# Performance work log

Measured on AMD Instinct MI355X. Metric: run time of the kernel, lower is better.

## Reference

```python
import jax, jax.numpy as jnp
import numpy as np

D_K = 64  # matches init_kwargs d_k


def setup_inputs() -> dict:
    key = jax.random.key(0)
    k0, k1, k2, k3 = jax.random.split(key, 4)
    B, H, TW, L, D = 4, 8, 20, 256, 64
    q = jax.random.normal(k0, (B, H, TW, D), dtype=jnp.float32)
    k = jax.random.normal(k1, (B, H, L, D), dtype=jnp.float32)
    v = jax.random.normal(k2, (B, H, L, D), dtype=jnp.float32)
    bias = jax.random.normal(k3, (B, L, H, TW, L), dtype=jnp.float32)
    return {"q": q, "k": k, "v": v, "bias": bias}


def reference(q, k, v, bias):
    # q: [B,H,TW,D]; k,v: [B,H,L,D]; bias: [B,L,H,TW,L]
    B, H, TW, D = q.shape
    L = k.shape[2]
    # The torch code expands q over the L axis before matmul with k^T; since
    # QK^T does not depend on that axis, compute it once and broadcast.
    scores = jnp.einsum('bhwd,bhld->bhwl', q, k) / jnp.sqrt(jnp.asarray(D_K, q.dtype))
    # weight: [B,L,H,TW,L]; dropout-before-softmax is identity in eval mode
    w = jax.nn.softmax(scores[:, None, :, :, :] + bias, axis=-1)
    # transpose(1,2).view(B,H,L*TW,L) @ v, then transpose(1,2).view(B,L*TW,H*D)
    attn = jnp.einsum('blhwk,bhkd->blwhd', w, v)  # [B,L,TW,H,D]
    return attn.reshape(B, L * TW, H * D)
```

## Files before the change

kernel.cpp:

```cpp
#include <hip/hip_runtime.h>
#include <hip/hip_bf16.h>

#define NB 4
#define NH 8
#define NW 20
#define NL 256
#define ND 64
#define ROWGRPS 40

typedef __attribute__((ext_vector_type(8))) short bf16x8;
typedef __attribute__((ext_vector_type(4))) short short4v;
typedef __attribute__((ext_vector_type(4))) float f32x4;

static __device__ __forceinline__ short f2bf(float f) {
  __hip_bfloat16 h = __float2bfloat16(f);
  short s;
  __builtin_memcpy(&s, &h, 2);
  return s;
}
static __device__ __forceinline__ float bf2f(short s) {
  __hip_bfloat16 h;
  __builtin_memcpy(&h, &s, 2);
  return __bfloat162float(h);
}

__global__ __launch_bounds__(256) void qk_scores_kernel(
    const float* __restrict__ q, const float* __restrict__ k,
    float* __restrict__ scores) {
  const int bid = blockIdx.x;
  const int w = bid % NW;
  const int bh = bid / NW;
  const int l = threadIdx.x;
  const f32x4* qrow = (const f32x4*)(q + ((long)bh * NW + w) * ND);
  const f32x4* krow = (const f32x4*)(k + ((long)bh * NL + l) * ND);
  float acc = 0.f;
#pragma unroll
  for (int j = 0; j < ND / 4; ++j) {
    f32x4 a = qrow[j];
    f32x4 c = krow[j];
    acc += a.x * c.x + a.y * c.y + a.z * c.z + a.w * c.w;
  }
  scores[((long)bh * NW + w) * NL + l] = acc * 0.125f;
}

__global__ __launch_bounds__(512, 5) void attn_kernel(
    const float* __restrict__ v, const float* __restrict__ bias,
    const float* __restrict__ scores, float* __restrict__ out) {
  __shared__ short sv_hi[128 * ND];
  __shared__ short sv_lo[128 * ND];

  const int t = threadIdx.x;
  const int bid = blockIdx.x;
  const int rg = bid % ROWGRPS;
  const int h = (bid / ROWGRPS) % NH;
  const int b = bid / (ROWGRPS * NH);

  const int wave = t >> 6;
  const int lane = t & 63;
  const int rl = lane & 15;
  const int g = lane >> 4;
  const int r0 = rg * 128 + wave * 16;
  const int row = r0 + rl;
  const int li = row / NW;
  const int wi = row % NW;

  const float* brow = bias + (((long)(b * NL + li) * NH + h) * NW + wi) * NL;
  const float* srow = scores + ((long)((b * NH + h) * NW + wi)) * NL;

  const int sd = t & 63;
  const int kb4 = (t >> 6) * 4;
  const float* vbase = v + ((long)(b * NH + h)) * NL * ND + sd;
  auto stage = [&](int kh) {
    const float* vp = vbase + (long)(kh * 128) * ND;
#pragma unroll
    for (int i = 0; i < 4; ++i) {
      const int kl = kb4 + i * 32;
      float f0 = vp[(long)(kl + 0) * ND];
      float f1 = vp[(long)(kl + 1) * ND];
      float f2 = vp[(long)(kl + 2) * ND];
      float f3 = vp[(long)(kl + 3) * ND];
      short4v hi, lo;
      hi.x = f2bf(f0); lo.x = f2bf(f0 - bf2f(hi.x));
      hi.y = f2bf(f1); lo.y = f2bf(f1 - bf2f(hi.y));
      hi.z = f2bf(f2); lo.z = f2bf(f2 - bf2f(hi.z));
      hi.w = f2bf(f3); lo.w = f2bf(f3 - bf2f(hi.w));
      const int off = (sd << 8) + ((kl << 1) ^ ((sd & 7) << 4));
      *(short4v*)((char*)sv_hi + off) = hi;
      *(short4v*)((char*)sv_lo + off) = lo;
    }
  };

  f32x4 nb0, nb1, ns0, ns1;
  auto issue = [&](int s) {
    const float* bp = brow + s * 32 + g * 8;
    const float* sp = srow + s * 32 + g * 8;
    nb0 = __builtin_nontemporal_load((const f32x4*)bp);
    nb1 = __builtin_nontemporal_load((const f32x4*)(bp + 4));
    ns0 = *(const f32x4*)sp;
    ns1 = *(const f32x4*)(sp + 4);
  };

  f32x4 acc[4];
#pragma unroll
  for (int dt = 0; dt < 4; ++dt) acc[dt] = (f32x4){0.f, 0.f, 0.f, 0.f};
  float den = 0.f;

  const char* hb = (const char*)sv_hi;
  const char* lb = (const char*)sv_lo;

  auto body = [&](int sl, f32x4 b0, f32x4 b1, f32x4 s0, f32x4 s1) {
    float p[8];
    p[0] = __expf(b0.x + s0.x);
    p[1] = __expf(b0.y + s0.y);
    p[2] = __expf(b0.z + s0.z);
    p[3] = __expf(b0.w + s0.w);
    p[4] = __expf(b1.x + s1.x);
    p[5] = __expf(b1.y + s1.y);
    p[6] = __expf(b1.z + s1.z);
    p[7] = __expf(b1.w + s1.w);
    den += ((p[0] + p[1]) + (p[2] + p[3])) + ((p[4] + p[5]) + (p[6] + p[7]));
    bf16x8 phi, plo;
#pragma unroll
    for (int j = 0; j < 8; ++j) {
      short hj = f2bf(p[j]);
      phi[j] = hj;
      plo[j] = f2bf(p[j] - bf2f(hj));
    }
    const int k0l = sl * 32 + g * 8;
#pragma unroll
    for (int dt = 0; dt < 4; ++dt) {
      const int d = dt * 16 + rl;
      const int off = (d << 8) + ((k0l << 1) ^ ((d & 7) << 4));
      bf16x8 vh = *(const bf16x8*)(hb + off);
      bf16x8 vl = *(const bf16x8*)(lb + off);
      acc[dt] = __builtin_amdgcn_mfma_f32_16x16x32_bf16(phi, vh, acc[dt], 0, 0, 0);
      acc[dt] = __builtin_amdgcn_mfma_f32_16x16x32_bf16(phi, vl, acc[dt], 0, 0, 0);
      acc[dt] = __builtin_amdgcn_mfma_f32_16x16x32_bf16(plo, vh, acc[dt], 0, 0, 0);
    }
  };

  issue(0);
  stage(0);
  __syncthreads();
#pragma unroll
  for (int s = 0; s < 4; ++s) {
    f32x4 b0 = nb0, b1 = nb1, s0 = ns0, s1 = ns1;
    issue(s + 1);
    body(s, b0, b1, s0, s1);
  }
  __syncthreads();
  stage(1);
  __syncthreads();
#pragma unroll
  for (int s = 4; s < 8; ++s) {
    f32x4 b0 = nb0, b1 = nb1, s0 = ns0, s1 = ns1;
    if (s < 7) issue(s + 1);
    body(s - 4, b0, b1, s0, s1);
  }

  float dsum = den + __shfl_xor(den, 16);
  dsum += __shfl_xor(dsum, 32);

  float* ob = out + ((long)b * (NL * NW)) * (NH * ND) + h * ND + rl;
#pragma unroll
  for (int i = 0; i < 4; ++i) {
    const int crow = (lane >> 4) * 4 + i;
    const float rinv = 1.0f / __shfl(dsum, crow);
    float* op = ob + (long)(r0 + crow) * (NH * ND);
    __builtin_nontemporal_store(acc[0][i] * rinv, op);
    __builtin_nontemporal_store(acc[1][i] * rinv, op + 16);
    __builtin_nontemporal_store(acc[2][i] * rinv, op + 32);
    __builtin_nontemporal_store(acc[3][i] * rinv, op + 48);
  }
}

extern "C" void kernel_launch(void* const* d_in, const int* in_sizes, int n_in,
                              void* d_out, int out_size, void* d_ws, size_t ws_size,
                              hipStream_t stream) {
  (void)in_sizes; (void)n_in; (void)out_size; (void)ws_size;
  const float* q = (const float*)d_in[0];
  const float* k = (const float*)d_in[1];
  const float* v = (const float*)d_in[2];
  const float* bias = (const float*)d_in[3];
  float* out = (float*)d_out;
  float* scores = (float*)d_ws;

  qk_scores_kernel<<<NB * NH * NW, NL, 0, stream>>>(q, k, scores);
  attn_kernel<<<NB * NH * ROWGRPS, 512, 0, stream>>>(v, bias, scores, out);
}
```

Baseline: 301.2 us.

## Halve attention block size and deepen bias prefetch to two stages ahead

Attention blocks now cover 64 rows with 256 threads instead of 128 rows with 512 threads, doubling the grid. V staging is adjusted so four waves fill the same shared tile. The bias and score loads move to a three-slot register ring that is issued two steps ahead, so more memory traffic is in flight. Output stores change from nontemporal to ordinary stores. Smaller blocks mean each block converts V to hi/lo bf16 for fewer rows, so that conversion work is repeated more often per row of output.

```diff
diff --git a/kernel.cpp b/kernel.cpp
--- a/kernel.cpp
+++ b/kernel.cpp
@@ -6,7 +6,7 @@
 #define NW 20
 #define NL 256
 #define ND 64
-#define ROWGRPS 40
+#define ROWGRPS 80
 
 typedef __attribute__((ext_vector_type(8))) short bf16x8;
 typedef __attribute__((ext_vector_type(4))) short short4v;
@@ -43,7 +43,7 @@
   scores[((long)bh * NW + w) * NL + l] = acc * 0.125f;
 }
 
-__global__ __launch_bounds__(512, 5) void attn_kernel(
+__global__ __launch_bounds__(256, 4) void attn_kernel(
     const float* __restrict__ v, const float* __restrict__ bias,
     const float* __restrict__ scores, float* __restrict__ out) {
   __shared__ short sv_hi[128 * ND];
@@ -59,7 +59,7 @@
   const int lane = t & 63;
   const int rl = lane & 15;
   const int g = lane >> 4;
-  const int r0 = rg * 128 + wave * 16;
+  const int r0 = rg * 64 + wave * 16;
   const int row = r0 + rl;
   const int li = row / NW;
   const int wi = row % NW;
@@ -68,13 +68,13 @@
   const float* srow = scores + ((long)((b * NH + h) * NW + wi)) * NL;
 
   const int sd = t & 63;
-  const int kb4 = (t >> 6) * 4;
+  const int kb = (t >> 6) * 4;
   const float* vbase = v + ((long)(b * NH + h)) * NL * ND + sd;
   auto stage = [&](int kh) {
     const float* vp = vbase + (long)(kh * 128) * ND;
 #pragma unroll
-    for (int i = 0; i < 4; ++i) {
-      const int kl = kb4 + i * 32;
+    for (int i = 0; i < 8; ++i) {
+      const int kl = kb + i * 16;
       float f0 = vp[(long)(kl + 0) * ND];
       float f1 = vp[(long)(kl + 1) * ND];
       float f2 = vp[(long)(kl + 2) * ND];
@@ -90,14 +90,14 @@
     }
   };
 
-  f32x4 nb0, nb1, ns0, ns1;
-  auto issue = [&](int s) {
+  f32x4 pb0[3], pb1[3], ps0[3], ps1[3];
+  auto issue = [&](int slot, int s) {
     const float* bp = brow + s * 32 + g * 8;
     const float* sp = srow + s * 32 + g * 8;
-    nb0 = __builtin_nontemporal_load((const f32x4*)bp);
-    nb1 = __builtin_nontemporal_load((const f32x4*)(bp + 4));
-    ns0 = *(const f32x4*)sp;
-    ns1 = *(const f32x4*)(sp + 4);
+    pb0[slot] = __builtin_nontemporal_load((const f32x4*)bp);
+    pb1[slot] = __builtin_nontemporal_load((const f32x4*)(bp + 4));
+    ps0[slot] = *(const f32x4*)sp;
+    ps1[slot] = *(const f32x4*)(sp + 4);
   };
 
   f32x4 acc[4];
@@ -139,23 +139,19 @@
     }
   };
 
-  issue(0);
+  issue(0, 0);
+  issue(1, 1);
   stage(0);
   __syncthreads();
 #pragma unroll
-  for (int s = 0; s < 4; ++s) {
-    f32x4 b0 = nb0, b1 = nb1, s0 = ns0, s1 = ns1;
-    issue(s + 1);
-    body(s, b0, b1, s0, s1);
-  }
-  __syncthreads();
-  stage(1);
-  __syncthreads();
-#pragma unroll
-  for (int s = 4; s < 8; ++s) {
-    f32x4 b0 = nb0, b1 = nb1, s0 = ns0, s1 = ns1;
-    if (s < 7) issue(s + 1);
-    body(s - 4, b0, b1, s0, s1);
+  for (int s = 0; s < 8; ++s) {
+    if (s == 4) {
+      __syncthreads();
+      stage(1);
+      __syncthreads();
+    }
+    if (s + 2 < 8) issue((s + 2) % 3, s + 2);
+    body(s & 3, pb0[s % 3], pb1[s % 3], ps0[s % 3], ps1[s % 3]);
   }
 
   float dsum = den + __shfl_xor(den, 16);
@@ -167,10 +163,10 @@
     const int crow = (lane >> 4) * 4 + i;
     const float rinv = 1.0f / __shfl(dsum, crow);
     float* op = ob + (long)(r0 + crow) * (NH * ND);
-    __builtin_nontemporal_store(acc[0][i] * rinv, op);
-    __builtin_nontemporal_store(acc[1][i] * rinv, op + 16);
-    __builtin_nontemporal_store(acc[2][i] * rinv, op + 32);
-    __builtin_nontemporal_store(acc[3][i] * rinv, op + 48);
+    op[0]  = acc[0][i] * rinv;
+    op[16] = acc[1][i] * rinv;
+    op[32] = acc[2][i] * rinv;
+    op[48] = acc[3][i] * rinv;
   }
 }
 
@@ -186,5 +182,5 @@
   float* scores = (float*)d_ws;
 
   qk_scores_kernel<<<NB * NH * NW, NL, 0, stream>>>(q, k, scores);
-  attn_kernel<<<NB * NH * ROWGRPS, 512, 0, stream>>>(v, bias, scores, out);
+  attn_kernel<<<NB * NH * ROWGRPS, 256, 0, stream>>>(v, bias, scores, out);
 }
```

After: 280.9 us. -6.7%, faster.
